# Kernel tuning notes

Hardware: AMD Instinct MI355X
Metric: run time of the kernel (lower is better)

## Reference

```python
import jax, jax.numpy as jnp
import numpy as np

D_MODEL = 1024
N_HEADS = 16
HEAD_DIM = D_MODEL // N_HEADS
B, S = 4, 2048


def setup_inputs() -> dict:
    key = jax.random.key(0)
    ks = jax.random.split(key, 9)
    sd = 1.0 / np.sqrt(D_MODEL)
    x = jax.random.normal(ks[0], (B, S, D_MODEL), dtype=jnp.float32)
    wq = jax.random.uniform(ks[1], (D_MODEL, D_MODEL), jnp.float32, -sd, sd)
    bq = jax.random.uniform(ks[2], (D_MODEL,), jnp.float32, -sd, sd)
    wk = jax.random.uniform(ks[3], (HEAD_DIM, D_MODEL), jnp.float32, -sd, sd)
    bk = jax.random.uniform(ks[4], (HEAD_DIM,), jnp.float32, -sd, sd)
    wv = jax.random.uniform(ks[5], (HEAD_DIM, D_MODEL), jnp.float32, -sd, sd)
    bv = jax.random.uniform(ks[6], (HEAD_DIM,), jnp.float32, -sd, sd)
    wo = jax.random.uniform(ks[7], (D_MODEL, D_MODEL), jnp.float32, -sd, sd)
    bo = jax.random.uniform(ks[8], (D_MODEL,), jnp.float32, -sd, sd)
    return {"x": x, "wq": wq, "bq": bq, "wk": wk, "bk": bk,
            "wv": wv, "bv": bv, "wo": wo, "bo": bo}


def reference(x, wq, bq, wk, bk, wv, bv, wo, bo):
    b, s, _ = x.shape
    scale = HEAD_DIM ** -0.5
    # projections (torch Linear: x @ W.T + b)
    q = (x @ wq.T + bq).reshape(b, s, N_HEADS, HEAD_DIM)  # [B,S,H,Dh]
    k = x @ wk.T + bk  # [B,S,Dh] single shared KV head
    v = x @ wv.T + bv  # [B,S,Dh]
    # QK^T with broadcast K: [B,H,S,S]
    attn = jnp.einsum('bqhd,bkd->bhqk', q, k) * scale
    attn = jax.nn.softmax(attn, axis=-1)
    # attend with broadcast V: [B,H,S,Dh]
    out = jnp.einsum('bhqk,bkd->bqhd', attn, v).reshape(b, s, D_MODEL)
    return out @ wo.T + bo
```

## Files before the change

kernel.cpp:

```cpp
#include <hip/hip_runtime.h>
#include <hip/hip_bf16.h>

#define D_MODEL 1024
#define HEAD_DIM 64
#define N_HEADS 16
#define BATCH 4
#define SEQ 2048
#define M_TOK (BATCH * SEQ)
#define N_QKV 1152

typedef unsigned short u16;
typedef unsigned int u32;
typedef __attribute__((ext_vector_type(8))) short s8;
typedef __attribute__((ext_vector_type(4))) float f4;
typedef __attribute__((ext_vector_type(16))) float f16x;

#define SCALE_LOG2E 0.18033688011112042f

__device__ __forceinline__ u16 f2bf(float f) {
    union { float f; unsigned u; } x; x.f = f;
    unsigned r = x.u + 0x7fffu + ((x.u >> 16) & 1u);
    return (u16)(r >> 16);
}

__device__ __forceinline__ u32 cvt_pk_bf16(float lo, float hi) {
    u32 r;
    asm("v_cvt_pk_bf16_f32 %0, %1, %2" : "=v"(r) : "v"(lo), "v"(hi));
    return r;
}

__global__ void cast_bf16(const float* __restrict__ in, u16* __restrict__ out, int n4) {
    int i = blockIdx.x * 256 + threadIdx.x;
    if (i < n4) {
        float4 v = reinterpret_cast<const float4*>(in)[i];
        ushort4 o;
        o.x = f2bf(v.x); o.y = f2bf(v.y); o.z = f2bf(v.z); o.w = f2bf(v.w);
        reinterpret_cast<ushort4*>(out)[i] = o;
    }
}

__global__ void cast_wcat(const float* __restrict__ wq, const float* __restrict__ wk,
                          const float* __restrict__ wv, u16* __restrict__ wcat) {
    int row = blockIdx.x, t = threadIdx.x;
    const float* src = (row < 1024) ? wq + (size_t)row * 1024
                     : (row < 1088) ? wk + (size_t)(row - 1024) * 1024
                                    : wv + (size_t)(row - 1088) * 1024;
    float4 v = reinterpret_cast<const float4*>(src)[t];
    ushort4 o;
    o.x = f2bf(v.x); o.y = f2bf(v.y); o.z = f2bf(v.z); o.w = f2bf(v.w);
    reinterpret_cast<ushort4*>(wcat + (size_t)row * 1024)[t] = o;
}

template<int MODE>
__global__ __launch_bounds__(256, 2)
void gemm_mfma_bt(const u16* __restrict__ A, const u16* __restrict__ B,
                  const float* __restrict__ bias0,
                  const float* __restrict__ bk_, const float* __restrict__ bv_,
                  void* __restrict__ C0, u16* __restrict__ kbf,
                  u16* __restrict__ vtb, int M, int N, int K)
{
    __shared__ u16 As[128 * 64];
    __shared__ u16 Bs[128 * 64];
    const int t = threadIdx.x;
    const int lane = t & 63, wid = t >> 6;
    const int lr = lane & 15, lg = lane >> 4;
    const int wm = wid >> 1, wn = wid & 1;
    const int bm = blockIdx.y * 128, bn = blockIdx.x * 128;

    f4 acc[4][4];
#pragma unroll
    for (int i = 0; i < 4; ++i)
#pragma unroll
        for (int j = 0; j < 4; ++j) acc[i][j] = (f4){0.f, 0.f, 0.f, 0.f};

    int srow[4], sseg[4], sdst[4];
#pragma unroll
    for (int i = 0; i < 4; ++i) {
        int c = t + i * 256;
        srow[i] = c >> 3; sseg[i] = c & 7;
        sdst[i] = srow[i] * 128 + ((sseg[i] * 16) ^ ((srow[i] & 7) << 4));
    }

    const int NT = K >> 6;
    s8 pa[4], pb[4];
#pragma unroll
    for (int i = 0; i < 4; ++i) {
        pa[i] = *(const s8*)(A + (size_t)(bm + srow[i]) * K + sseg[i] * 8);
        pb[i] = *(const s8*)(B + (size_t)(bn + srow[i]) * K + sseg[i] * 8);
    }

    for (int kt = 0; kt < NT; ++kt) {
        __syncthreads();
#pragma unroll
        for (int i = 0; i < 4; ++i) {
            *(s8*)((char*)As + sdst[i]) = pa[i];
            *(s8*)((char*)Bs + sdst[i]) = pb[i];
        }
        __syncthreads();
        if (kt + 1 < NT) {
            int k0 = (kt + 1) << 6;
#pragma unroll
            for (int i = 0; i < 4; ++i) {
                pa[i] = *(const s8*)(A + (size_t)(bm + srow[i]) * K + k0 + sseg[i] * 8);
                pb[i] = *(const s8*)(B + (size_t)(bn + srow[i]) * K + k0 + sseg[i] * 8);
            }
        }
#pragma unroll
        for (int kbk = 0; kbk < 2; ++kbk) {
            s8 af[4];
#pragma unroll
            for (int rb = 0; rb < 4; ++rb) {
                int row = wm * 64 + rb * 16 + lr;
                af[rb] = *(const s8*)((const char*)As + row * 128 +
                                      ((kbk * 64 + lg * 16) ^ ((row & 7) << 4)));
            }
#pragma unroll
            for (int cb = 0; cb < 4; ++cb) {
                int rowb = wn * 64 + cb * 16 + lr;
                s8 bf = *(const s8*)((const char*)Bs + rowb * 128 +
                                     ((kbk * 64 + lg * 16) ^ ((rowb & 7) << 4)));
#pragma unroll
                for (int rb = 0; rb < 4; ++rb)
                    acc[rb][cb] = __builtin_amdgcn_mfma_f32_16x16x32_bf16(
                        af[rb], bf, acc[rb][cb], 0, 0, 0);
            }
        }
    }

#pragma unroll
    for (int cb = 0; cb < 4; ++cb) {
        int col = bn + wn * 64 + cb * 16 + lr;
        float bb;
        if (MODE == 0) bb = bias0[col];
        else bb = (col < 1024) ? bias0[col]
                : (col < 1088) ? bk_[col - 1024] : bv_[col - 1088];
#pragma unroll
        for (int rb = 0; rb < 4; ++rb)
#pragma unroll
            for (int r = 0; r < 4; ++r) {
                int row = bm + wm * 64 + rb * 16 + lg * 4 + r;
                float v = acc[rb][cb][r] + bb;
                if (MODE == 0) {
                    ((float*)C0)[(size_t)row * 1024 + col] = v;
                } else {
                    if (col < 1024)
                        ((u16*)C0)[(size_t)row * 1024 + col] = f2bf(v * SCALE_LOG2E);
                    else if (col < 1088)
                        kbf[(size_t)row * HEAD_DIM + (col - 1024)] = f2bf(v);
                    else
                        vtb[((size_t)(row >> 11) * 64 + (col - 1088)) * SEQ +
                            (row & 2047)] = f2bf(v);
                }
            }
    }
}

__global__ __launch_bounds__(256, 4)
void mqa_flash_mfma(const u16* __restrict__ qb, const u16* __restrict__ kbuf,
                    const u16* __restrict__ vtb, u16* __restrict__ ob)
{
    __shared__ u16 Ks[64 * 64];
    __shared__ u16 Vts[64 * 64];
    const int t = threadIdx.x, lane = t & 63, wid = t >> 6;
    const int l31 = lane & 31, hi = lane >> 5;
    const int qt = blockIdx.x, h = blockIdx.y, b = blockIdx.z;
    const int q0 = qt * 128 + wid * 32;

    const u16* qbase = qb + (size_t)b * SEQ * D_MODEL + h * HEAD_DIM;
    const u16* kbase = kbuf + (size_t)b * SEQ * HEAD_DIM;
    const u16* vbase = vtb + (size_t)b * HEAD_DIM * SEQ;

    s8 qf[4];
#pragma unroll
    for (int s = 0; s < 4; ++s)
        qf[s] = *(const s8*)(qbase + (size_t)(q0 + l31) * D_MODEL + s * 16 + hi * 8);

    s8 ones;
#pragma unroll
    for (int j = 0; j < 8; ++j) ones[j] = (short)0x3F80;

    f16x oacc[2], oaccS;
#pragma unroll
    for (int r = 0; r < 16; ++r) { oacc[0][r] = 0.f; oacc[1][r] = 0.f; oaccS[r] = 0.f; }

    const int c0 = t, c1 = t + 256;
    const int r0 = c0 >> 3, s0 = c0 & 7, r1 = c1 >> 3, s1 = c1 & 7;
    const int d0 = r0 * 128 + ((s0 * 16) ^ ((r0 & 7) << 4));
    const int d1 = r1 * 128 + ((s1 * 16) ^ ((r1 & 7) << 4));

    s8 pk0 = *(const s8*)(kbase + (size_t)r0 * HEAD_DIM + s0 * 8);
    s8 pk1 = *(const s8*)(kbase + (size_t)r1 * HEAD_DIM + s1 * 8);
    s8 pv0 = *(const s8*)(vbase + (size_t)r0 * SEQ + s0 * 8);
    s8 pv1 = *(const s8*)(vbase + (size_t)r1 * SEQ + s1 * 8);

    const int swz = (l31 & 7) << 4;

    for (int kt = 0; kt < SEQ / 64; ++kt) {
        __syncthreads();
        *(s8*)((char*)Ks + d0) = pk0;  *(s8*)((char*)Ks + d1) = pk1;
        *(s8*)((char*)Vts + d0) = pv0; *(s8*)((char*)Vts + d1) = pv1;
        __syncthreads();
        if (kt + 1 < SEQ / 64) {
            int kt0 = (kt + 1) * 64;
            pk0 = *(const s8*)(kbase + (size_t)(kt0 + r0) * HEAD_DIM + s0 * 8);
            pk1 = *(const s8*)(kbase + (size_t)(kt0 + r1) * HEAD_DIM + s1 * 8);
            pv0 = *(const s8*)(vbase + (size_t)r0 * SEQ + kt0 + s0 * 8);
            pv1 = *(const s8*)(vbase + (size_t)r1 * SEQ + kt0 + s1 * 8);
        }

        f16x st[2];
#pragma unroll
        for (int kb = 0; kb < 2; ++kb) {
#pragma unroll
            for (int r = 0; r < 16; ++r) st[kb][r] = 0.f;
#pragma unroll
            for (int s = 0; s < 4; ++s) {
                s8 kf = *(const s8*)((const char*)Ks + (kb * 32 + l31) * 128 +
                                     ((s * 32 + hi * 16) ^ swz));
                st[kb] = __builtin_amdgcn_mfma_f32_32x32x16_bf16(
                    kf, qf[s], st[kb], 0, 0, 0);
            }
        }

        u32 pw[4][4];
#pragma unroll
        for (int kb = 0; kb < 2; ++kb)
#pragma unroll
            for (int sub = 0; sub < 2; ++sub) {
                float c[8];
#pragma unroll
                for (int i = 0; i < 8; ++i)
                    c[i] = exp2f(st[kb][sub * 8 + i]);
                u32 A = cvt_pk_bf16(c[0], c[1]);
                u32 B = cvt_pk_bf16(c[2], c[3]);
                u32 C = cvt_pk_bf16(c[4], c[5]);
                u32 D = cvt_pk_bf16(c[6], c[7]);
                asm("v_permlane32_swap_b32 %0, %1" : "+v"(A), "+v"(C));
                asm("v_permlane32_swap_b32 %0, %1" : "+v"(B), "+v"(D));
                int s = kb * 2 + sub;
                pw[s][0] = A; pw[s][1] = B; pw[s][2] = C; pw[s][3] = D;
            }

#pragma unroll
        for (int s = 0; s < 4; ++s) {
            s8 paf = *(const s8*)&pw[s][0];
#pragma unroll
            for (int dh = 0; dh < 2; ++dh) {
                s8 vf = *(const s8*)((const char*)Vts + (dh * 32 + l31) * 128 +
                                     ((s * 32 + hi * 16) ^ swz));
                oacc[dh] = __builtin_amdgcn_mfma_f32_32x32x16_bf16(
                    paf, vf, oacc[dh], 0, 0, 0);
            }
            oaccS = __builtin_amdgcn_mfma_f32_32x32x16_bf16(
                paf, ones, oaccS, 0, 0, 0);
        }
    }

    u16* obase = ob + (size_t)b * SEQ * D_MODEL + h * HEAD_DIM;
#pragma unroll
    for (int r = 0; r < 16; ++r) {
        float inv = 1.f / oaccS[r];
        int qrow = (r & 3) + 8 * (r >> 2) + 4 * hi;
        int row = q0 + qrow;
#pragma unroll
        for (int dh = 0; dh < 2; ++dh)
            obase[(size_t)row * D_MODEL + dh * 32 + l31] =
                f2bf(oacc[dh][r] * inv);
    }
}

extern "C" void kernel_launch(void* const* d_in, const int* in_sizes, int n_in,
                              void* d_out, int out_size, void* d_ws, size_t ws_size,
                              hipStream_t stream)
{
    const float* x  = (const float*)d_in[0];
    const float* wq = (const float*)d_in[1];
    const float* bq = (const float*)d_in[2];
    const float* wk = (const float*)d_in[3];
    const float* bk = (const float*)d_in[4];
    const float* wv = (const float*)d_in[5];
    const float* bv = (const float*)d_in[6];
    const float* wo = (const float*)d_in[7];
    const float* bo = (const float*)d_in[8];
    float* out = (float*)d_out;

    u16* base = (u16*)d_ws;
    u16* xbf  = base;
    u16* qbuf = xbf  + (size_t)M_TOK * D_MODEL;
    u16* abuf = qbuf + (size_t)M_TOK * D_MODEL;
    u16* kbf  = abuf + (size_t)M_TOK * D_MODEL;
    u16* vtb  = kbf  + (size_t)M_TOK * HEAD_DIM;
    u16* wcat = vtb  + (size_t)M_TOK * HEAD_DIM;
    u16* wob  = wcat + (size_t)N_QKV * D_MODEL;

    cast_bf16<<<(M_TOK * D_MODEL / 4 + 255) / 256, 256, 0, stream>>>(
        x, xbf, M_TOK * D_MODEL / 4);
    cast_wcat<<<N_QKV, 256, 0, stream>>>(wq, wk, wv, wcat);
    cast_bf16<<<(D_MODEL * D_MODEL / 4 + 255) / 256, 256, 0, stream>>>(
        wo, wob, D_MODEL * D_MODEL / 4);

    gemm_mfma_bt<1><<<dim3(N_QKV / 128, M_TOK / 128), 256, 0, stream>>>(
        xbf, wcat, bq, bk, bv, qbuf, kbf, vtb, M_TOK, N_QKV, D_MODEL);

    mqa_flash_mfma<<<dim3(SEQ / 128, N_HEADS, BATCH), 256, 0, stream>>>(
        qbuf, kbf, vtb, abuf);

    gemm_mfma_bt<0><<<dim3(D_MODEL / 128, M_TOK / 128), 256, 0, stream>>>(
        abuf, wob, bo, nullptr, nullptr, out, nullptr, nullptr,
        M_TOK, D_MODEL, D_MODEL);
}
```

Before: 175.7 us.

## Raise wave priority around MFMA blocks, merge weight casts, unroll attention loop

Brackets the MFMA sections of both the GEMM and the flash-attention kernel with s_setprio so that waves issuing matrix ops get scheduling priority over waves doing loads and exp. Merges the Wo cast into the QKV weight-cast kernel to save one launch. The attention loop is unrolled by two, and the first score MFMA now takes a zero vector as its accumulator instead of zeroing st each iteration. Together these aim to cut launch overhead and improve overlap between MFMA and the other work, at the cost of more register pressure from the unroll.

```diff
diff --git a/kernel.cpp b/kernel.cpp
--- a/kernel.cpp
+++ b/kernel.cpp
@@ -39,16 +39,20 @@
     }
 }
 
-__global__ void cast_wcat(const float* __restrict__ wq, const float* __restrict__ wk,
-                          const float* __restrict__ wv, u16* __restrict__ wcat) {
+__global__ void cast_weights(const float* __restrict__ wq, const float* __restrict__ wk,
+                             const float* __restrict__ wv, const float* __restrict__ wo,
+                             u16* __restrict__ wcat, u16* __restrict__ wob) {
     int row = blockIdx.x, t = threadIdx.x;
-    const float* src = (row < 1024) ? wq + (size_t)row * 1024
-                     : (row < 1088) ? wk + (size_t)(row - 1024) * 1024
-                                    : wv + (size_t)(row - 1088) * 1024;
+    const float* src;
+    u16* dst;
+    if (row < 1024)      { src = wq + (size_t)row * 1024;          dst = wcat + (size_t)row * 1024; }
+    else if (row < 1088) { src = wk + (size_t)(row - 1024) * 1024; dst = wcat + (size_t)row * 1024; }
+    else if (row < 1152) { src = wv + (size_t)(row - 1088) * 1024; dst = wcat + (size_t)row * 1024; }
+    else                 { src = wo + (size_t)(row - 1152) * 1024; dst = wob + (size_t)(row - 1152) * 1024; }
     float4 v = reinterpret_cast<const float4*>(src)[t];
     ushort4 o;
     o.x = f2bf(v.x); o.y = f2bf(v.y); o.z = f2bf(v.z); o.w = f2bf(v.w);
-    reinterpret_cast<ushort4*>(wcat + (size_t)row * 1024)[t] = o;
+    reinterpret_cast<ushort4*>(dst)[t] = o;
 }
 
 template<int MODE>
@@ -105,6 +109,7 @@
                 pb[i] = *(const s8*)(B + (size_t)(bn + srow[i]) * K + k0 + sseg[i] * 8);
             }
         }
+        __builtin_amdgcn_s_setprio(1);
 #pragma unroll
         for (int kbk = 0; kbk < 2; ++kbk) {
             s8 af[4];
@@ -125,6 +130,7 @@
                         af[rb], bf, acc[rb][cb], 0, 0, 0);
             }
         }
+        __builtin_amdgcn_s_setprio(0);
     }
 
 #pragma unroll
@@ -179,6 +185,10 @@
 #pragma unroll
     for (int j = 0; j < 8; ++j) ones[j] = (short)0x3F80;
 
+    f16x z16;
+#pragma unroll
+    for (int r = 0; r < 16; ++r) z16[r] = 0.f;
+
     f16x oacc[2], oaccS;
 #pragma unroll
     for (int r = 0; r < 16; ++r) { oacc[0][r] = 0.f; oacc[1][r] = 0.f; oaccS[r] = 0.f; }
@@ -195,6 +205,7 @@
 
     const int swz = (l31 & 7) << 4;
 
+#pragma unroll 2
     for (int kt = 0; kt < SEQ / 64; ++kt) {
         __syncthreads();
         *(s8*)((char*)Ks + d0) = pk0;  *(s8*)((char*)Ks + d1) = pk1;
@@ -209,18 +220,24 @@
         }
 
         f16x st[2];
+        __builtin_amdgcn_s_setprio(1);
 #pragma unroll
         for (int kb = 0; kb < 2; ++kb) {
-#pragma unroll
-            for (int r = 0; r < 16; ++r) st[kb][r] = 0.f;
-#pragma unroll
-            for (int s = 0; s < 4; ++s) {
+            {
+                s8 kf = *(const s8*)((const char*)Ks + (kb * 32 + l31) * 128 +
+                                     ((0 * 32 + hi * 16) ^ swz));
+                st[kb] = __builtin_amdgcn_mfma_f32_32x32x16_bf16(
+                    kf, qf[0], z16, 0, 0, 0);
+            }
+#pragma unroll
+            for (int s = 1; s < 4; ++s) {
                 s8 kf = *(const s8*)((const char*)Ks + (kb * 32 + l31) * 128 +
                                      ((s * 32 + hi * 16) ^ swz));
                 st[kb] = __builtin_amdgcn_mfma_f32_32x32x16_bf16(
                     kf, qf[s], st[kb], 0, 0, 0);
             }
         }
+        __builtin_amdgcn_s_setprio(0);
 
         u32 pw[4][4];
 #pragma unroll
@@ -241,6 +258,7 @@
                 pw[s][0] = A; pw[s][1] = B; pw[s][2] = C; pw[s][3] = D;
             }
 
+        __builtin_amdgcn_s_setprio(1);
 #pragma unroll
         for (int s = 0; s < 4; ++s) {
             s8 paf = *(const s8*)&pw[s][0];
@@ -254,6 +272,7 @@
             oaccS = __builtin_amdgcn_mfma_f32_32x32x16_bf16(
                 paf, ones, oaccS, 0, 0, 0);
         }
+        __builtin_amdgcn_s_setprio(0);
     }
 
     u16* obase = ob + (size_t)b * SEQ * D_MODEL + h * HEAD_DIM;
@@ -295,9 +314,7 @@
 
     cast_bf16<<<(M_TOK * D_MODEL / 4 + 255) / 256, 256, 0, stream>>>(
         x, xbf, M_TOK * D_MODEL / 4);
-    cast_wcat<<<N_QKV, 256, 0, stream>>>(wq, wk, wv, wcat);
-    cast_bf16<<<(D_MODEL * D_MODEL / 4 + 255) / 256, 256, 0, stream>>>(
-        wo, wob, D_MODEL * D_MODEL / 4);
+    cast_weights<<<N_QKV + 1024, 256, 0, stream>>>(wq, wk, wv, wo, wcat, wob);
 
     gemm_mfma_bt<1><<<dim3(N_QKV / 128, M_TOK / 128), 256, 0, stream>>>(
         xbf, wcat, bq, bk, bv, qbuf, kbf, vtb, M_TOK, N_QKV, D_MODEL);
```

Result: slower. 252.0 us (+43.4%).
